# Kernel tuning notes

Measured on AMD Instinct MI355X. Metric: run time of the kernel, lower is better.

The kernel has to match this reference:

```python
import jax, jax.numpy as jnp
import numpy as np


def setup_inputs() -> dict:
    key = jax.random.key(0)
    k1, k2, k3 = jax.random.split(key, 3)
    N, C, V, T, K = 32, 64, 25, 1024, 3
    x = jax.random.normal(k1, (N, C, V, T), dtype=jnp.float32)
    # grouped 1x1 conv weight: per node v, maps C -> K*C. torch weight (C*K*V, C, 1, 1)
    W = jax.random.normal(k2, (V, K * C, C), dtype=jnp.float32) * 0.05
    # adjacency buffer A[k, w, v] (src node w -> dst node v, partition k)
    A = jax.random.uniform(k3, (K, V, V), dtype=jnp.float32)
    return {"x": x, "W": W, "A": A}


def reference(x, W, A):
    # x: [N, C, V, T]; W: [V, K*C, C]; A: [K, V, V]
    N, C, V, T = x.shape
    K = A.shape[0]
    # permute(0,2,1,3): [N, V, C, T]; grouped 1x1 conv == per-node matmul C -> K*C
    y = jnp.einsum('ncvt,voc->nvot', x, W)          # [N, V, K*C, T]
    # view (N, V, C*K, T) with output-channel layout o = c*K + k -> split to (C, K)
    y = y.reshape(N, V, C, K, T)                     # [N, V(src=w), C, K, T]
    # einsum('kwv,nckwt->ncvt')
    out = jnp.einsum('kwv,nwckt->ncvt', A, y)        # [N, C, V, T]
    return out
```

## Files before the change

### kernel.cpp

```cpp
#include <hip/hip_runtime.h>

#define Nn 32
#define Cc 64
#define Vv 25
#define Tt 1024

typedef __attribute__((ext_vector_type(4))) float f32x4;
typedef __attribute__((ext_vector_type(8))) short bf16x8;
typedef __attribute__((ext_vector_type(4))) unsigned short u16x4;

__device__ __forceinline__ unsigned short f2bf(float f) {
    union { float f; unsigned u; } a; a.f = f;
    unsigned u = a.u;
    u += 0x7fff + ((u >> 16) & 1);
    return (unsigned short)(u >> 16);
}

__device__ __forceinline__ void gl_lds16(const unsigned short* g, unsigned short* l) {
    __builtin_amdgcn_global_load_lds(
        (const __attribute__((address_space(1))) unsigned int*)g,
        (__attribute__((address_space(3))) unsigned int*)l, 16, 0, 0);
}


__global__ __launch_bounds__(256) void weff_prep_sw(
        const float* __restrict__ W, const float* __restrict__ A,
        unsigned short* __restrict__ Weff) {
    int v = blockIdx.x / Vv;
    int w = blockIdx.x - v * Vv;
    float a0 = A[(0 * Vv + w) * Vv + v];
    float a1 = A[(1 * Vv + w) * Vv + v];
    float a2 = A[(2 * Vv + w) * Vv + v];
    const float* Wb = W + (size_t)w * 192 * 64;
    unsigned short* o = Weff + (size_t)(v * Vv + w) * 4096;
    int c  = threadIdx.x >> 2;
    int c0 = (threadIdx.x & 3) * 16;
    #pragma unroll
    for (int i = 0; i < 16; ++i) {
        int cp = c0 + i;
        float val = a0 * Wb[(c * 3 + 0) * 64 + cp]
                  + a1 * Wb[(c * 3 + 1) * 64 + cp]
                  + a2 * Wb[(c * 3 + 2) * 64 + cp];
        int jl = cp >> 3;
        o[c * 64 + ((jl ^ (c & 7)) << 3) + (cp & 7)] = f2bf(val);
    }
}

__global__ __launch_bounds__(256) void x_convert(
        const float* __restrict__ x, unsigned short* __restrict__ xb) {
    __shared__ __align__(16) unsigned short tile[64 * 64];
    int bid = blockIdx.x;
    int n = bid / (Vv * 16);
    int rem = bid - n * (Vv * 16);
    int w = rem >> 4;
    int t0 = (rem & 15) << 6;
    int tid = threadIdx.x;
    int g = tid & 15, q = tid >> 4;
    const float* xp = x + ((size_t)(n * Cc) * Vv + w) * Tt + t0 + q * 4;
    f32x4 f[4];
    #pragma unroll
    for (int cj = 0; cj < 4; ++cj)
        f[cj] = *(const f32x4*)(xp + (size_t)(g * 4 + cj) * Vv * Tt);
    #pragma unroll
    for (int r = 0; r < 4; ++r) {
        int t = q * 4 + r;
        u16x4 h = { f2bf(f[0][r]), f2bf(f[1][r]), f2bf(f[2][r]), f2bf(f[3][r]) };
        int pc = (g >> 1) ^ (t & 7);
        *(u16x4*)&tile[t * 64 + pc * 8 + (g & 1) * 4] = h;
    }
    __syncthreads();
    unsigned short* dst = xb + ((size_t)(n * Vv + w) * Tt + t0) * 64;
    #pragma unroll
    for (int r = 0; r < 2; ++r) {
        int fo = tid * 16 + r * 8;
        *(bf16x8*)&dst[fo] = *(const bf16x8*)&tile[fo];
    }
}

__global__ __launch_bounds__(256, 2) void gc_fast(
        const unsigned short* __restrict__ xb,
        const unsigned short* __restrict__ Weff,
        float* __restrict__ out) {
    __shared__ __align__(16) unsigned short wa[3][4096];

    int bid = blockIdx.x;
    int xcd = bid & 7;
    int lid = bid >> 3;
    int v = lid % Vv;
    int s = lid / Vv;
    int slice = (xcd << 4) + s;
    int n  = slice >> 2;
    int t0 = (slice & 3) << 8;

    int tid = threadIdx.x;
    int lane = tid & 63, wv = tid >> 6;
    int m = lane & 15, quad = lane >> 4;

    const unsigned short* wg = Weff + (size_t)v * (Vv * 4096);
    const unsigned short* xbase = xb + ((size_t)(n * Vv) * Tt + t0) * 64;

    int coff0 = ((quad)     ^ (m & 7)) << 3;
    int coff1 = ((4 + quad) ^ (m & 7)) << 3;
    int trow[4], arow[4];
    #pragma unroll
    for (int ni = 0; ni < 4; ++ni) trow[ni] = (wv * 64 + ni * 16 + m) * 64;
    #pragma unroll
    for (int mi = 0; mi < 4; ++mi) arow[mi] = (mi * 16 + m) * 64;

    f32x4 acc[4][4];
    #pragma unroll
    for (int i = 0; i < 4; ++i)
        #pragma unroll
        for (int j = 0; j < 4; ++j)
            acc[i][j] = (f32x4){0.f, 0.f, 0.f, 0.f};

    bf16x8 bA[8], bB[8];

#define ISSUE_A(WBUF, w_) do { \
    const unsigned short* s_ = wg + (size_t)(w_) * 4096 + tid * 8; \
    gl_lds16(s_,        &wa[WBUF][tid * 8]); \
    gl_lds16(s_ + 2048, &wa[WBUF][2048 + tid * 8]); \
} while (0)

#define ISSUE_B(BN, w_) do { \
    const unsigned short* xw_ = xbase + (size_t)(w_) * (Tt * 64); \
    _Pragma("unroll") \
    for (int ni_ = 0; ni_ < 4; ++ni_) { \
        BN[ni_]     = *(const bf16x8*)(xw_ + trow[ni_] + coff0); \
        BN[ni_ + 4] = *(const bf16x8*)(xw_ + trow[ni_] + coff1); \
    } \
} while (0)

#define COMPUTE(RBUF, BC) do { \
    const unsigned short* cur_ = &wa[RBUF][0]; \
    bf16x8 af_[8]; \
    _Pragma("unroll") \
    for (int mi_ = 0; mi_ < 4; ++mi_) { \
        af_[mi_]     = *(const bf16x8*)(cur_ + arow[mi_] + coff0); \
        af_[mi_ + 4] = *(const bf16x8*)(cur_ + arow[mi_] + coff1); \
    } \
    __builtin_amdgcn_s_setprio(1); \
    _Pragma("unroll") \
    for (int mi_ = 0; mi_ < 4; ++mi_) \
        _Pragma("unroll") \
        for (int ni_ = 0; ni_ < 4; ++ni_) \
            acc[mi_][ni_] = __builtin_amdgcn_mfma_f32_16x16x32_bf16( \
                af_[mi_], BC[ni_], acc[mi_][ni_], 0, 0, 0); \
    _Pragma("unroll") \
    for (int mi_ = 0; mi_ < 4; ++mi_) \
        _Pragma("unroll") \
        for (int ni_ = 0; ni_ < 4; ++ni_) \
            acc[mi_][ni_] = __builtin_amdgcn_mfma_f32_16x16x32_bf16( \
                af_[mi_ + 4], BC[ni_ + 4], acc[mi_][ni_], 0, 0, 0); \
    __builtin_amdgcn_s_setprio(0); \
} while (0)

#define STEP(RBUF, WBUF, BC, BN, w_) do { \
    ISSUE_A(WBUF, (w_) + 1); \
    ISSUE_B(BN, (w_) + 1); \
    __builtin_amdgcn_sched_barrier(0); \
    asm volatile("s_waitcnt vmcnt(10)" ::: "memory"); \
    __builtin_amdgcn_sched_barrier(0); \
    __builtin_amdgcn_s_barrier(); \
    __builtin_amdgcn_sched_barrier(0); \
    COMPUTE(RBUF, BC); \
} while (0)

    ISSUE_A(0, 0);
    ISSUE_B(bA, 0);
    __builtin_amdgcn_sched_barrier(0);

    for (int t6 = 0; t6 < 4; ++t6) {
        int w0 = t6 * 6;
        STEP(0, 1, bA, bB, w0 + 0);
        STEP(1, 2, bB, bA, w0 + 1);
        STEP(2, 0, bA, bB, w0 + 2);
        STEP(0, 1, bB, bA, w0 + 3);
        STEP(1, 2, bA, bB, w0 + 4);
        STEP(2, 0, bB, bA, w0 + 5);
    }
    asm volatile("s_waitcnt vmcnt(0)" ::: "memory");
    __builtin_amdgcn_sched_barrier(0);
    __builtin_amdgcn_s_barrier();
    __builtin_amdgcn_sched_barrier(0);
    COMPUTE(0, bA);

#undef ISSUE_A
#undef ISSUE_B
#undef COMPUTE
#undef STEP

    float* og = out + ((size_t)n * Cc * Vv + v) * Tt + t0 + wv * 64 + m;
    #pragma unroll
    for (int mi = 0; mi < 4; ++mi)
        #pragma unroll
        for (int r = 0; r < 4; ++r) {
            int c = mi * 16 + quad * 4 + r;
            float* orow = og + (size_t)c * Vv * Tt;
            #pragma unroll
            for (int ni = 0; ni < 4; ++ni)
                orow[ni * 16] = acc[mi][ni][r];
        }
}


__global__ __launch_bounds__(256) void weff_prep_plain(
        const float* __restrict__ W, const float* __restrict__ A,
        unsigned short* __restrict__ Weff) {
    int v = blockIdx.x / Vv;
    int w = blockIdx.x - v * Vv;
    float a0 = A[(0 * Vv + w) * Vv + v];
    float a1 = A[(1 * Vv + w) * Vv + v];
    float a2 = A[(2 * Vv + w) * Vv + v];
    const float* Wb = W + (size_t)w * 192 * 64;
    unsigned short* o = Weff + (size_t)(v * Vv + w) * 4096;
    int e0 = threadIdx.x * 16;
    #pragma unroll
    for (int i = 0; i < 16; ++i) {
        int e = e0 + i;
        int c = e >> 6, cp = e & 63;
        float val = a0 * Wb[(c * 3 + 0) * 64 + cp]
                  + a1 * Wb[(c * 3 + 1) * 64 + cp]
                  + a2 * Wb[(c * 3 + 2) * 64 + cp];
        o[e] = f2bf(val);
    }
}

__global__ __launch_bounds__(256, 2) void gc_plain(
        const float* __restrict__ x, const unsigned short* __restrict__ Weff,
        float* __restrict__ out) {
    __shared__ __align__(16) unsigned short xs[256 * 72];
    __shared__ __align__(16) unsigned short wa[64 * 72];
    int bid = blockIdx.x;
    int xcd = bid & 7;
    int lid = bid >> 3;
    int v, s;
    if (lid < 13 * 16) { v = lid % 13;            s = lid / 13; }
    else { int l2 = lid - 13 * 16; v = 13 + l2 % 12; s = l2 / 12; }
    int slice = (xcd << 4) + s;
    int n  = slice >> 2;
    int t0 = (slice & 3) << 8;
    int tid  = threadIdx.x;
    int lane = tid & 63;
    int wv   = tid >> 6;
    int m    = lane & 15;
    int quad = lane >> 4;
    int cc = tid & 7;
    int tt = tid >> 3;
    f32x4 acc[4][4];
    #pragma unroll
    for (int i = 0; i < 4; ++i)
        #pragma unroll
        for (int j = 0; j < 4; ++j)
            acc[i][j] = (f32x4){0.f, 0.f, 0.f, 0.f};
    const float* xg = x + (size_t)n * Cc * Vv * Tt + t0 + tt * 4;
    const bf16x8* wg = (const bf16x8*)(Weff + (size_t)v * Vv * 4096);
    for (int w = 0; w < Vv; ++w) {
        if (w) __syncthreads();
        #pragma unroll
        for (int r = 0; r < 2; ++r) {
            int q = r * 256 + tid;
            int c = q >> 3, b = q & 7;
            *(bf16x8*)&wa[c * 72 + b * 8] = wg[w * 512 + q];
        }
        {
            bf16x8 rows[8];
            #pragma unroll
            for (int i = 0; i < 8; ++i) {
                int cp = cc * 8 + i;
                const float* p = xg + ((size_t)cp * Vv + w) * Tt;
                float4 f0 = *(const float4*)p;
                float4 f1 = *(const float4*)(p + 128);
                rows[0][i] = (short)f2bf(f0.x); rows[1][i] = (short)f2bf(f0.y);
                rows[2][i] = (short)f2bf(f0.z); rows[3][i] = (short)f2bf(f0.w);
                rows[4][i] = (short)f2bf(f1.x); rows[5][i] = (short)f2bf(f1.y);
                rows[6][i] = (short)f2bf(f1.z); rows[7][i] = (short)f2bf(f1.w);
            }
            #pragma unroll
            for (int j = 0; j < 4; ++j) {
                *(bf16x8*)&xs[(tt * 4 + j) * 72 + cc * 8]       = rows[j];
                *(bf16x8*)&xs[(128 + tt * 4 + j) * 72 + cc * 8] = rows[4 + j];
            }
        }
        __syncthreads();
        #pragma unroll
        for (int kc = 0; kc < 2; ++kc) {
            int ko = kc * 32 + quad * 8;
            bf16x8 afr[4], bfr[4];
            #pragma unroll
            for (int mi = 0; mi < 4; ++mi)
                afr[mi] = *(const bf16x8*)&wa[(mi * 16 + m) * 72 + ko];
            #pragma unroll
            for (int ni = 0; ni < 4; ++ni)
                bfr[ni] = *(const bf16x8*)&xs[(wv * 64 + ni * 16 + m) * 72 + ko];
            #pragma unroll
            for (int mi = 0; mi < 4; ++mi)
                #pragma unroll
                for (int ni = 0; ni < 4; ++ni)
                    acc[mi][ni] = __builtin_amdgcn_mfma_f32_16x16x32_bf16(
                        afr[mi], bfr[ni], acc[mi][ni], 0, 0, 0);
        }
    }
    float* og = out + ((size_t)n * Cc * Vv + v) * Tt + t0 + wv * 64 + m;
    #pragma unroll
    for (int mi = 0; mi < 4; ++mi)
        #pragma unroll
        for (int r = 0; r < 4; ++r) {
            int c = mi * 16 + quad * 4 + r;
            float* orow = og + (size_t)c * Vv * Tt;
            #pragma unroll
            for (int ni = 0; ni < 4; ++ni)
                orow[ni * 16] = acc[mi][ni][r];
        }
}

extern "C" void kernel_launch(void* const* d_in, const int* in_sizes, int n_in,
                              void* d_out, int out_size, void* d_ws, size_t ws_size,
                              hipStream_t stream) {
    const float* x = (const float*)d_in[0];
    const float* W = (const float*)d_in[1];
    const float* A = (const float*)d_in[2];
    float* out = (float*)d_out;

    const size_t xb_elems   = (size_t)Nn * Vv * Tt * 64;
    const size_t weff_elems = (size_t)Vv * Vv * 4096;
    const size_t need = (xb_elems + weff_elems) * sizeof(unsigned short);

    if (ws_size >= need) {
        unsigned short* xb   = (unsigned short*)d_ws;
        unsigned short* Weff = xb + xb_elems;
        weff_prep_sw<<<dim3(Vv * Vv), dim3(256), 0, stream>>>(W, A, Weff);
        x_convert<<<dim3(Nn * Vv * 16), dim3(256), 0, stream>>>(x, xb);
        gc_fast<<<dim3(3200), dim3(256), 0, stream>>>(xb, Weff, out);
    } else {
        unsigned short* Weff = (unsigned short*)d_ws;
        weff_prep_plain<<<dim3(Vv * Vv), dim3(256), 0, stream>>>(W, A, Weff);
        gc_plain<<<dim3(3200), dim3(256), 0, stream>>>(x, Weff, out);
    }
}
```

Baseline: 563.4 us.

## Fuse prep kernels and deepen gc_fast pipeline to prefetch distance two

Merges the weight-fold and x-to-bf16 conversion kernels into one launch, with larger 256-timestep tiles and nontemporal loads of x. The main kernel moves from triple-buffered to quad-buffered LDS weights with three register sets for x fragments, prefetching two node steps ahead with a relaxed waitcnt. Output stores become nontemporal. The aim is to hide more memory latency and cut launch overhead, at the cost of more LDS and VGPR use, which may lower occupancy.

```diff
diff --git a/kernel.cpp b/kernel.cpp
--- a/kernel.cpp
+++ b/kernel.cpp
@@ -23,57 +23,64 @@
 }
 
 
-__global__ __launch_bounds__(256) void weff_prep_sw(
-        const float* __restrict__ W, const float* __restrict__ A,
+__global__ __launch_bounds__(256) void prep_fused(
+        const float* __restrict__ x, const float* __restrict__ W,
+        const float* __restrict__ A, unsigned short* __restrict__ xb,
         unsigned short* __restrict__ Weff) {
-    int v = blockIdx.x / Vv;
-    int w = blockIdx.x - v * Vv;
-    float a0 = A[(0 * Vv + w) * Vv + v];
-    float a1 = A[(1 * Vv + w) * Vv + v];
-    float a2 = A[(2 * Vv + w) * Vv + v];
-    const float* Wb = W + (size_t)w * 192 * 64;
-    unsigned short* o = Weff + (size_t)(v * Vv + w) * 4096;
-    int c  = threadIdx.x >> 2;
-    int c0 = (threadIdx.x & 3) * 16;
+    int bid = blockIdx.x;
+    if (bid < Vv * Vv) {
+        int v = bid / Vv;
+        int w = bid - v * Vv;
+        float a0 = A[(0 * Vv + w) * Vv + v];
+        float a1 = A[(1 * Vv + w) * Vv + v];
+        float a2 = A[(2 * Vv + w) * Vv + v];
+        const float* Wb = W + (size_t)w * 192 * 64;
+        unsigned short* o = Weff + (size_t)(v * Vv + w) * 4096;
+        int c  = threadIdx.x >> 2;
+        int c0 = (threadIdx.x & 3) * 16;
+        #pragma unroll
+        for (int i = 0; i < 16; ++i) {
+            int cp = c0 + i;
+            float val = a0 * Wb[(c * 3 + 0) * 64 + cp]
+                      + a1 * Wb[(c * 3 + 1) * 64 + cp]
+                      + a2 * Wb[(c * 3 + 2) * 64 + cp];
+            int jl = cp >> 3;
+            o[c * 64 + ((jl ^ (c & 7)) << 3) + (cp & 7)] = f2bf(val);
+        }
+        return;
+    }
+    __shared__ __align__(16) unsigned short tile[256 * 64];
+    int pid = bid - Vv * Vv;
+    int n = pid / (Vv * 4);
+    int rem = pid - n * (Vv * 4);
+    int w = rem >> 2;
+    int t0 = (rem & 3) << 8;
+
+    int tid = threadIdx.x;
+    int wv = tid >> 6;
+    int l  = tid & 63;
+    int sr = l >> 4;
+    int tc = l & 15;
+
+    const float* xn = x + ((size_t)n * Cc * Vv + w) * Tt + t0 + wv * 64 + tc * 4;
     #pragma unroll
     for (int i = 0; i < 16; ++i) {
-        int cp = c0 + i;
-        float val = a0 * Wb[(c * 3 + 0) * 64 + cp]
-                  + a1 * Wb[(c * 3 + 1) * 64 + cp]
-                  + a2 * Wb[(c * 3 + 2) * 64 + cp];
-        int jl = cp >> 3;
-        o[c * 64 + ((jl ^ (c & 7)) << 3) + (cp & 7)] = f2bf(val);
-    }
-}
-
-__global__ __launch_bounds__(256) void x_convert(
-        const float* __restrict__ x, unsigned short* __restrict__ xb) {
-    __shared__ __align__(16) unsigned short tile[64 * 64];
-    int bid = blockIdx.x;
-    int n = bid / (Vv * 16);
-    int rem = bid - n * (Vv * 16);
-    int w = rem >> 4;
-    int t0 = (rem & 15) << 6;
-    int tid = threadIdx.x;
-    int g = tid & 15, q = tid >> 4;
-    const float* xp = x + ((size_t)(n * Cc) * Vv + w) * Tt + t0 + q * 4;
-    f32x4 f[4];
-    #pragma unroll
-    for (int cj = 0; cj < 4; ++cj)
-        f[cj] = *(const f32x4*)(xp + (size_t)(g * 4 + cj) * Vv * Tt);
-    #pragma unroll
-    for (int r = 0; r < 4; ++r) {
-        int t = q * 4 + r;
-        u16x4 h = { f2bf(f[0][r]), f2bf(f[1][r]), f2bf(f[2][r]), f2bf(f[3][r]) };
-        int pc = (g >> 1) ^ (t & 7);
-        *(u16x4*)&tile[t * 64 + pc * 8 + (g & 1) * 4] = h;
+        int r = i * 4 + sr;
+        const f32x4* p = (const f32x4*)(xn + (size_t)r * (Vv * Tt));
+        f32x4 f = __builtin_nontemporal_load(p);
+        #pragma unroll
+        for (int j = 0; j < 4; ++j) {
+            int tl = wv * 64 + tc * 4 + j;
+            int pc = (r >> 3) ^ (tl & 7);
+            tile[tl * 64 + pc * 8 + (r & 7)] = f2bf(f[j]);
+        }
     }
     __syncthreads();
     unsigned short* dst = xb + ((size_t)(n * Vv + w) * Tt + t0) * 64;
     #pragma unroll
-    for (int r = 0; r < 2; ++r) {
-        int fo = tid * 16 + r * 8;
-        *(bf16x8*)&dst[fo] = *(const bf16x8*)&tile[fo];
+    for (int rr = 0; rr < 8; ++rr) {
+        int u = rr * 256 + tid;
+        *(bf16x8*)&dst[u * 8] = *(const bf16x8*)&tile[u * 8];
     }
 }
 
@@ -81,7 +88,7 @@
         const unsigned short* __restrict__ xb,
         const unsigned short* __restrict__ Weff,
         float* __restrict__ out) {
-    __shared__ __align__(16) unsigned short wa[3][4096];
+    __shared__ __align__(16) unsigned short wa[4][4096];
 
     int bid = blockIdx.x;
     int xcd = bid & 7;
@@ -114,7 +121,7 @@
         for (int j = 0; j < 4; ++j)
             acc[i][j] = (f32x4){0.f, 0.f, 0.f, 0.f};
 
-    bf16x8 bA[8], bB[8];
+    bf16x8 b0[8], b1[8], b2[8];
 
 #define ISSUE_A(WBUF, w_) do { \
     const unsigned short* s_ = wg + (size_t)(w_) * 4096 + tid * 8; \
@@ -155,35 +162,56 @@
     __builtin_amdgcn_s_setprio(0); \
 } while (0)
 
-#define STEP(RBUF, WBUF, BC, BN, w_) do { \
-    ISSUE_A(WBUF, (w_) + 1); \
-    ISSUE_B(BN, (w_) + 1); \
+#define STEP(RB, WB, BC, BN, w_) do { \
+    ISSUE_A(WB, (w_) + 2); \
+    ISSUE_B(BN, (w_) + 2); \
     __builtin_amdgcn_sched_barrier(0); \
-    asm volatile("s_waitcnt vmcnt(10)" ::: "memory"); \
+    asm volatile("s_waitcnt vmcnt(20)" ::: "memory"); \
     __builtin_amdgcn_sched_barrier(0); \
     __builtin_amdgcn_s_barrier(); \
     __builtin_amdgcn_sched_barrier(0); \
-    COMPUTE(RBUF, BC); \
+    COMPUTE(RB, BC); \
 } while (0)
 
     ISSUE_A(0, 0);
-    ISSUE_B(bA, 0);
-    __builtin_amdgcn_sched_barrier(0);
-
-    for (int t6 = 0; t6 < 4; ++t6) {
-        int w0 = t6 * 6;
-        STEP(0, 1, bA, bB, w0 + 0);
-        STEP(1, 2, bB, bA, w0 + 1);
-        STEP(2, 0, bA, bB, w0 + 2);
-        STEP(0, 1, bB, bA, w0 + 3);
-        STEP(1, 2, bA, bB, w0 + 4);
-        STEP(2, 0, bB, bA, w0 + 5);
-    }
+    ISSUE_B(b0, 0);
+    ISSUE_A(1, 1);
+    ISSUE_B(b1, 1);
+    __builtin_amdgcn_sched_barrier(0);
+
+    STEP(0, 2, b0, b2,  0);
+    STEP(1, 3, b1, b0,  1);
+    STEP(2, 0, b2, b1,  2);
+    STEP(3, 1, b0, b2,  3);
+    STEP(0, 2, b1, b0,  4);
+    STEP(1, 3, b2, b1,  5);
+    STEP(2, 0, b0, b2,  6);
+    STEP(3, 1, b1, b0,  7);
+    STEP(0, 2, b2, b1,  8);
+    STEP(1, 3, b0, b2,  9);
+    STEP(2, 0, b1, b0, 10);
+    STEP(3, 1, b2, b1, 11);
+    STEP(0, 2, b0, b2, 12);
+    STEP(1, 3, b1, b0, 13);
+    STEP(2, 0, b2, b1, 14);
+    STEP(3, 1, b0, b2, 15);
+    STEP(0, 2, b1, b0, 16);
+    STEP(1, 3, b2, b1, 17);
+    STEP(2, 0, b0, b2, 18);
+    STEP(3, 1, b1, b0, 19);
+    STEP(0, 2, b2, b1, 20);
+    STEP(1, 3, b0, b2, 21);
+    STEP(2, 0, b1, b0, 22);
+    asm volatile("s_waitcnt vmcnt(10)" ::: "memory");
+    __builtin_amdgcn_sched_barrier(0);
+    __builtin_amdgcn_s_barrier();
+    __builtin_amdgcn_sched_barrier(0);
+    COMPUTE(3, b2);
     asm volatile("s_waitcnt vmcnt(0)" ::: "memory");
     __builtin_amdgcn_sched_barrier(0);
     __builtin_amdgcn_s_barrier();
     __builtin_amdgcn_sched_barrier(0);
-    COMPUTE(0, bA);
+    COMPUTE(0, b0);
 
 #undef ISSUE_A
 #undef ISSUE_B
@@ -199,7 +227,7 @@
             float* orow = og + (size_t)c * Vv * Tt;
             #pragma unroll
             for (int ni = 0; ni < 4; ++ni)
-                orow[ni * 16] = acc[mi][ni][r];
+                __builtin_nontemporal_store(acc[mi][ni][r], &orow[ni * 16]);
         }
 }
 
@@ -329,8 +357,7 @@
     if (ws_size >= need) {
         unsigned short* xb   = (unsigned short*)d_ws;
         unsigned short* Weff = xb + xb_elems;
-        weff_prep_sw<<<dim3(Vv * Vv), dim3(256), 0, stream>>>(W, A, Weff);
-        x_convert<<<dim3(Nn * Vv * 16), dim3(256), 0, stream>>>(x, xb);
+        prep_fused<<<dim3(Vv * Vv + Nn * Vv * 4), dim3(256), 0, stream>>>(x, W, A, xb, Weff);
         gc_fast<<<dim3(3200), dim3(256), 0, stream>>>(xb, Weff, out);
     } else {
         unsigned short* Weff = (unsigned short*)d_ws;
```

After: 500.7 us. 11.1% less time.
